# Performance work log

Hardware: AMD Instinct MI355X
Metric: run time of the kernel (lower is better)

## Reference

```python
import jax, jax.numpy as jnp
import numpy as np
from jax import lax

# Static problem sizes (see shape_source): 128 events x 512 points each
G, P, K = 128, 512, 16          # graphs, points per graph, knn k
FEAT = 128                       # n_samples*2
PLANES = [128, 96, 64, 32]       # linear reduction, n_graph=3, graph_out=32
N_OUT = 3                        # n_type


def setup_inputs() -> dict:
    key = jax.random.key(0)
    ks = jax.random.split(key, 24)
    N = G * P
    x = jax.random.normal(ks[0], (N, FEAT), jnp.float32)
    # coo: integer detector coords (cols 0,1) + graph id (col 2)
    xy = jax.random.randint(ks[1], (N, 2), 0, 32).astype(jnp.int32)
    gid = jnp.repeat(jnp.arange(G, dtype=jnp.int32), P)
    coo = jnp.concatenate([xy, gid[:, None]], axis=1)  # [N,3]
    inp = {"x": x, "coo": coo}
    # SAGEConv params per layer: lin_l (neighbor-mean path, with bias), lin_r (root path)
    ki = 2
    for l, (nin, nout) in enumerate(zip(PLANES[:-1], PLANES[1:])):
        s = 1.0 / np.sqrt(nin)
        inp[f"wl{l}"] = jax.random.normal(ks[ki], (nin, nout), jnp.float32) * s; ki += 1
        inp[f"wr{l}"] = jax.random.normal(ks[ki], (nin, nout), jnp.float32) * s; ki += 1
        inp[f"b{l}"] = jnp.zeros((nout,), jnp.float32)
    # MLP head: 32 -> 32 -> 3 with ReLU between (n_lin = 2)
    inp["lw0"] = jax.random.normal(ks[ki], (PLANES[-1], PLANES[-1]), jnp.float32) / np.sqrt(PLANES[-1]); ki += 1
    inp["lb0"] = jnp.zeros((PLANES[-1],), jnp.float32)
    inp["lw1"] = jax.random.normal(ks[ki], (PLANES[-1], N_OUT), jnp.float32) / np.sqrt(PLANES[-1]); ki += 1
    inp["lb1"] = jnp.zeros((N_OUT,), jnp.float32)
    return inp


def _knn_indices(coo):
    # knn_graph(coo, k, batch=coo[:,2], loop=False): k nearest within each graph,
    # self excluded. Batch segments are uniform size P so reshape per-graph.
    pos = coo.reshape(G, P, 3).astype(jnp.float32)
    d2 = jnp.sum((pos[:, :, None, :] - pos[:, None, :, :]) ** 2, axis=-1)  # [G,P,P]
    d2 = jnp.where(jnp.eye(P, dtype=bool), jnp.inf, d2)  # loop=False
    _, idx = lax.top_k(-d2, K)  # [G,P,K] neighbor (source) indices per target
    return idx


def reference(x, coo, wl0, wr0, b0, wl1, wr1, b1, wl2, wr2, b2, lw0, lb0, lw1, lb1):
    idx = _knn_indices(coo)
    h = x.reshape(G, P, FEAT)
    gather = jax.vmap(lambda hg, ig: hg[ig])  # per-graph neighbor gather
    for wl, wr, b in ((wl0, wr0, b0), (wl1, wr1, b1), (wl2, wr2, b2)):
        nbr_mean = gather(h, idx).mean(axis=2)  # [G,P,K,nin] -> [G,P,nin]
        # SAGEConv: lin_l(mean_j x_j) + lin_r(x_i), then ReLU (GraphLayer)
        h = jax.nn.relu(jnp.einsum('gpi,io->gpo', nbr_mean, wl)
                        + jnp.einsum('gpi,io->gpo', h, wr) + b)
    pooled = h.max(axis=1)  # global_max_pool over batch -> [G, 32]
    hid = jax.nn.relu(pooled @ lw0 + lb0)
    return hid @ lw1 + lb1  # [G, 3]
```

## Files before the change

kernel.cpp:

```cpp
#include <hip/hip_runtime.h>

#define G 128
#define P 512
#define K 16
#define NPTS (G * P)

typedef _Float16 half8 __attribute__((ext_vector_type(8)));
typedef float    floatx4 __attribute__((ext_vector_type(4)));

__device__ __forceinline__ unsigned uminu(unsigned a, unsigned b) { return a < b ? a : b; }

__device__ __forceinline__ void ce(unsigned& a, unsigned& b) {
    const unsigned lo = a < b ? a : b;
    const unsigned hi = a < b ? b : a;
    a = lo; b = hi;
}

__device__ __forceinline__ void sort16(unsigned k[16]) {
#pragma unroll
    for (int p = 1; p < 16; p <<= 1) {
#pragma unroll
        for (int q = p; q >= 1; q >>= 1) {
#pragma unroll
            for (int j = q % p; j + q < 16; j += 2 * q) {
#pragma unroll
                for (int i = 0; i < q; ++i) {
                    const int a = i + j, b2 = i + j + q;
                    if (b2 < 16 && (a / (2 * p)) == (b2 / (2 * p)))
                        ce(k[a], k[b2]);
                }
            }
        }
    }
}

__device__ __forceinline__ void halfmerge(unsigned best[16], const unsigned kb[16]) {
#pragma unroll
    for (int i = 0; i < 16; ++i) best[i] = uminu(best[i], kb[15 - i]);
#pragma unroll
    for (int d = 8; d >= 1; d >>= 1)
#pragma unroll
        for (int i = 0; i < 16; ++i)
            if ((i & d) == 0) ce(best[i], best[i + d]);
}

template <int KT, int NIN, int NOUT>
__device__ __forceinline__ void prep_elem(int e, const float* __restrict__ wl,
                                          const float* __restrict__ wr,
                                          _Float16* __restrict__ wf) {
    const int fr   = e >> 9;
    const int lane = (e >> 3) & 63;
    const int j    = e & 7;
    const int ntile = fr / KT;
    const int kt    = fr - ntile * KT;
    const int k = kt * 32 + ((lane >> 4) << 3) + j;
    const int n = ntile * 16 + (lane & 15);
    const float v = (k < NIN) ? wl[k * NOUT + n] : wr[(k - NIN) * NOUT + n];
    wf[e] = (_Float16)v;
}

__global__ __launch_bounds__(512, 4)
void pre_kernel(const int* __restrict__ coo, int* __restrict__ idx_out,
                const float* __restrict__ x, _Float16* __restrict__ x16,
                const float* __restrict__ wl0, const float* __restrict__ wr0,
                const float* __restrict__ wl1, const float* __restrict__ wr1,
                const float* __restrict__ wl2, const float* __restrict__ wr2,
                _Float16* __restrict__ wf0, _Float16* __restrict__ wf1,
                _Float16* __restrict__ wf2) {
    __shared__ float2 sxy[P];
    __shared__ unsigned mk[7][64][17];
    const int b   = blockIdx.x;
    const int tid = threadIdx.x;

    if (b < 1024) {
        const int g   = b >> 3;
        const int t0  = (b & 7) * 64;
        const int tgt = tid & 63;
        const int sub = tid >> 6;

        for (int i = tid; i < P; i += 512) {
            const int* cp = coo + (size_t)(g * P + i) * 3;
            sxy[i] = make_float2((float)cp[0], (float)cp[1]);
        }
        __syncthreads();

        const int tg = t0 + tgt;
        const float px = sxy[tg].x, py = sxy[tg].y;

        unsigned best[K];
#pragma unroll
        for (int k = 0; k < K; ++k) best[k] = 0xFFFFFFF0u + k;

        const int s0 = sub * 64;
#pragma unroll
        for (int batch = 0; batch < 4; ++batch) {
            unsigned kb[K];
#pragma unroll
            for (int j = 0; j < 16; ++j) {
                const int s = s0 + batch * 16 + j;
                const float2 c = sxy[s];
                const float dx = px - c.x, dy = py - c.y;
                const float keyf = fmaf(fmaf(dx, dx, dy * dy), 512.f, (float)s);
                unsigned key = (unsigned)keyf;
                if (s == tg) key = 0xFFFFFFFFu;
                kb[j] = key;
            }
            sort16(kb);
            halfmerge(best, kb);
        }

        if (sub != 0) {
#pragma unroll
            for (int k = 0; k < K; ++k) mk[sub - 1][tgt][k] = best[k];
        }
        __syncthreads();
        if (sub == 0) {
#pragma unroll 1
            for (int ss = 0; ss < 7; ++ss) {
                unsigned pb[K];
#pragma unroll
                for (int k = 0; k < K; ++k) pb[k] = mk[ss][tgt][k];
                halfmerge(best, pb);
            }
            int4* op = (int4*)(idx_out + (size_t)(g * P + tg) * K);
#pragma unroll
            for (int q4 = 0; q4 < 4; ++q4) {
                int4 o;
                o.x = (int)(best[q4 * 4 + 0] & (unsigned)(P - 1));
                o.y = (int)(best[q4 * 4 + 1] & (unsigned)(P - 1));
                o.z = (int)(best[q4 * 4 + 2] & (unsigned)(P - 1));
                o.w = (int)(best[q4 * 4 + 3] & (unsigned)(P - 1));
                op[q4] = o;
            }
        }
    } else if (b < 3072) {
        const int i = (b - 1024) * 512 + tid;
        const float4* p = (const float4*)(x + (size_t)i * 8);
        const float4 a = p[0], bq = p[1];
        half8 o;
        o[0] = (_Float16)a.x;  o[1] = (_Float16)a.y;
        o[2] = (_Float16)a.z;  o[3] = (_Float16)a.w;
        o[4] = (_Float16)bq.x; o[5] = (_Float16)bq.y;
        o[6] = (_Float16)bq.z; o[7] = (_Float16)bq.w;
        *(half8*)(x16 + (size_t)i * 8) = o;
    } else {
        const int e = (b - 3072) * 512 + tid;
        if (e < 24576)      prep_elem<8, 128, 96>(e,         wl0, wr0, wf0);
        else if (e < 36864) prep_elem<6,  96, 64>(e - 24576, wl1, wr1, wf1);
        else                prep_elem<4,  64, 32>(e - 36864, wl2, wr2, wf2);
    }
}

template <int CIN, int NOUT, bool POOL>
__global__ __launch_bounds__(256, 4)
void sage_kernel(const _Float16* __restrict__ hin, const int* __restrict__ idxg,
                 const _Float16* __restrict__ wf, const float* __restrict__ bias,
                 _Float16* __restrict__ hout, float* __restrict__ pool_part) {
    constexpr int KTm = CIN / 32;
    constexpr int KT  = CIN / 16;
    constexpr int NH  = NOUT / 32;
    constexpr int RS  = 136;

    __shared__ _Float16 As[64 * RS];

    const int tid  = threadIdx.x;
    const int b    = blockIdx.x;
    const int slot = b >> 3;
    const int g    = (b & 7) | ((slot & 15) << 3);
    const int chunk = slot >> 4;
    const int n0   = g * P + chunk * 64;
    const _Float16* __restrict__ hg = hin + (size_t)(g * P) * CIN;

    const int pt = tid >> 2;
    const int q  = tid & 3;

    const int4* ip = (const int4*)(idxg + (size_t)(n0 + pt) * K);
    const int4 na = ip[0], nb4 = ip[1], nc = ip[2], nd = ip[3];
    const int nn[16] = {na.x, na.y, na.z, na.w, nb4.x, nb4.y, nb4.z, nb4.w,
                        nc.x, nc.y, nc.z, nc.w, nd.x, nd.y, nd.z, nd.w};

#pragma unroll 1
    for (int c = 0; c < KTm; ++c) {
        const int ch = c * 32 + q * 8;
        half8 a0 = {}; half8 a1 = {};
#pragma unroll
        for (int k = 0; k < 16; k += 4) {
            const half8 v0 = *(const half8*)(hg + (size_t)nn[k + 0] * CIN + ch);
            const half8 v1 = *(const half8*)(hg + (size_t)nn[k + 1] * CIN + ch);
            const half8 v2 = *(const half8*)(hg + (size_t)nn[k + 2] * CIN + ch);
            const half8 v3 = *(const half8*)(hg + (size_t)nn[k + 3] * CIN + ch);
            a0 += v0; a1 += v1; a0 += v2; a1 += v3;
        }
        half8 m;
#pragma unroll
        for (int e = 0; e < 8; ++e)
            m[e] = (_Float16)(((float)a0[e] + (float)a1[e]) * 0.0625f);
        *(half8*)&As[pt * RS + (c * 4 + q) * 8] = m;
    }

    const int l  = tid & 63;
    const int wv = tid >> 6;
    const int mh = wv & 1;
    const int nh = wv >> 1;
    const int lm = l & 15, lq = l >> 4;

    float bs[NH];
#pragma unroll
    for (int nt = 0; nt < NH; ++nt)
        bs[nt] = bias[nh * (NOUT / 2) + nt * 16 + lm];

    __syncthreads();

    floatx4 acc[2][NH];
#pragma unroll
    for (int mt = 0; mt < 2; ++mt)
#pragma unroll
        for (int nt = 0; nt < NH; ++nt) {
            floatx4 z = {0.f, 0.f, 0.f, 0.f};
            acc[mt][nt] = z;
        }

#pragma unroll
    for (int kt = 0; kt < KT; ++kt) {
        half8 bfr[NH];
#pragma unroll
        for (int nt = 0; nt < NH; ++nt) {
            const int ng = nh * NH + nt;
            bfr[nt] = *(const half8*)(wf + ((size_t)(ng * KT + kt) * 64 + l) * 8);
        }
#pragma unroll
        for (int mt = 0; mt < 2; ++mt) {
            const int row = mh * 32 + mt * 16 + lm;
            half8 a;
            if (kt < KTm) {
                a = *(const half8*)&As[row * RS + (kt * 4 + lq) * 8];
            } else {
                a = *(const half8*)(hin + (size_t)(n0 + row) * CIN +
                                    (kt - KTm) * 32 + lq * 8);
            }
#pragma unroll
            for (int nt = 0; nt < NH; ++nt)
                acc[mt][nt] = __builtin_amdgcn_mfma_f32_16x16x32_f16(
                    a, bfr[nt], acc[mt][nt], 0, 0, 0);
        }
    }

    if constexpr (!POOL) {
#pragma unroll
        for (int mt = 0; mt < 2; ++mt)
#pragma unroll
            for (int nt = 0; nt < NH; ++nt) {
                const int n = nh * (NOUT / 2) + nt * 16 + lm;
#pragma unroll
                for (int r = 0; r < 4; ++r) {
                    const int p = n0 + mh * 32 + mt * 16 + lq * 4 + r;
                    float v = acc[mt][nt][r] + bs[nt];
                    v = v > 0.f ? v : 0.f;
                    hout[(size_t)p * NOUT + n] = (_Float16)v;
                }
            }
    } else {
        __shared__ float ps[4][16];
        float vmax = 0.f;
#pragma unroll
        for (int mt = 0; mt < 2; ++mt)
#pragma unroll
            for (int r = 0; r < 4; ++r)
                vmax = fmaxf(vmax, acc[mt][0][r] + bs[0]);
        vmax = fmaxf(vmax, __shfl_xor(vmax, 16, 64));
        vmax = fmaxf(vmax, __shfl_xor(vmax, 32, 64));
        if (lq == 0) ps[wv][lm] = vmax;
        __syncthreads();
        if (tid < 32) {
            const int nh2 = tid >> 4, lm2 = tid & 15;
            pool_part[(size_t)(g * 8 + chunk) * 32 + tid] =
                fmaxf(ps[nh2 * 2][lm2], ps[nh2 * 2 + 1][lm2]);
        }
    }
}

__global__ __launch_bounds__(64)
void head_kernel(const float* __restrict__ pool_part,
                 const float* __restrict__ lw0, const float* __restrict__ lb0,
                 const float* __restrict__ lw1, const float* __restrict__ lb1,
                 float* __restrict__ out) {
    __shared__ float pooled[32];
    __shared__ float hid[32];
    const int g = blockIdx.x;
    const int t = threadIdx.x;

    if (t < 32) {
        float m = pool_part[(size_t)(g * 8) * 32 + t];
#pragma unroll
        for (int c = 1; c < 8; ++c)
            m = fmaxf(m, pool_part[(size_t)(g * 8 + c) * 32 + t]);
        pooled[t] = m;
    }
    __syncthreads();
    if (t < 32) {
        float a = lb0[t];
#pragma unroll
        for (int i = 0; i < 32; ++i) a += pooled[i] * lw0[i * 32 + t];
        hid[t] = a > 0.f ? a : 0.f;
    }
    __syncthreads();
    if (t < 3) {
        float a = lb1[t];
#pragma unroll
        for (int i = 0; i < 32; ++i) a += hid[i] * lw1[i * 3 + t];
        out[g * 3 + t] = a;
    }
}

extern "C" void kernel_launch(void* const* d_in, const int* in_sizes, int n_in,
                              void* d_out, int out_size, void* d_ws, size_t ws_size,
                              hipStream_t stream) {
    const float* x   = (const float*)d_in[0];
    const int*   coo = (const int*)  d_in[1];
    const float* wl0 = (const float*)d_in[2];
    const float* wr0 = (const float*)d_in[3];
    const float* b0  = (const float*)d_in[4];
    const float* wl1 = (const float*)d_in[5];
    const float* wr1 = (const float*)d_in[6];
    const float* b1  = (const float*)d_in[7];
    const float* wl2 = (const float*)d_in[8];
    const float* wr2 = (const float*)d_in[9];
    const float* b2  = (const float*)d_in[10];
    const float* lw0 = (const float*)d_in[11];
    const float* lb0 = (const float*)d_in[12];
    const float* lw1 = (const float*)d_in[13];
    const float* lb1 = (const float*)d_in[14];
    float* out = (float*)d_out;

    char* ws = (char*)d_ws;
    _Float16* wf0 = (_Float16*)(ws + 0);
    _Float16* wf1 = (_Float16*)(ws + 49152);
    _Float16* wf2 = (_Float16*)(ws + 73728);
    int*      idx = (int*)     (ws + 81920);
    _Float16* x16 = (_Float16*)(ws + 4276224);
    _Float16* h1  = (_Float16*)(ws + 21053440);
    _Float16* h2  = (_Float16*)(ws + 33636352);
    float*    pool= (float*)   (ws + 42024960);

    pre_kernel<<<3152, 512, 0, stream>>>(coo, idx, x, x16,
                                         wl0, wr0, wl1, wr1, wl2, wr2,
                                         wf0, wf1, wf2);

    sage_kernel<128, 96, false><<<1024, 256, 0, stream>>>(x16, idx, wf0, b0, h1, nullptr);
    sage_kernel< 96, 64, false><<<1024, 256, 0, stream>>>(h1,  idx, wf1, b1, h2, nullptr);
    sage_kernel< 64, 32, true ><<<1024, 256, 0, stream>>>(h2,  idx, wf2, b2, nullptr, pool);

    head_kernel<<<G, 64, 0, stream>>>(pool, lw0, lb0, lw1, lb1, out);
}
```

Baseline: 162.5 us.

## Halve SAGE block tile to 32 points with 8 threads per point

Each SAGE block now handles 32 points instead of 64, with 8 threads per point splitting the channel groups during the neighbor-mean gather. Each wave owns a single 16-row MFMA tile. The grid doubles to 2048 blocks, launch bounds allow 8 blocks per CU, and pool partials grow to 16 chunks per graph. The aim is more parallelism and occupancy to hide gather latency. In exchange, weight fragments are reloaded twice as often per point and the per-thread work is smaller.

```diff
diff --git a/kernel.cpp b/kernel.cpp
--- a/kernel.cpp
+++ b/kernel.cpp
@@ -152,50 +152,55 @@
 }
 
 template <int CIN, int NOUT, bool POOL>
-__global__ __launch_bounds__(256, 4)
+__global__ __launch_bounds__(256, 8)
 void sage_kernel(const _Float16* __restrict__ hin, const int* __restrict__ idxg,
                  const _Float16* __restrict__ wf, const float* __restrict__ bias,
                  _Float16* __restrict__ hout, float* __restrict__ pool_part) {
     constexpr int KTm = CIN / 32;
     constexpr int KT  = CIN / 16;
     constexpr int NH  = NOUT / 32;
+    constexpr int NG  = CIN / 8;
+    constexpr int PASSES = (NG + 7) / 8;
     constexpr int RS  = 136;
 
-    __shared__ _Float16 As[64 * RS];
+    __shared__ _Float16 As[32 * RS];
 
     const int tid  = threadIdx.x;
     const int b    = blockIdx.x;
     const int slot = b >> 3;
     const int g    = (b & 7) | ((slot & 15) << 3);
     const int chunk = slot >> 4;
-    const int n0   = g * P + chunk * 64;
+    const int n0   = g * P + chunk * 32;
     const _Float16* __restrict__ hg = hin + (size_t)(g * P) * CIN;
 
-    const int pt = tid >> 2;
-    const int q  = tid & 3;
+    const int pt = tid >> 3;
+    const int q  = tid & 7;
 
     const int4* ip = (const int4*)(idxg + (size_t)(n0 + pt) * K);
     const int4 na = ip[0], nb4 = ip[1], nc = ip[2], nd = ip[3];
     const int nn[16] = {na.x, na.y, na.z, na.w, nb4.x, nb4.y, nb4.z, nb4.w,
                         nc.x, nc.y, nc.z, nc.w, nd.x, nd.y, nd.z, nd.w};
 
-#pragma unroll 1
-    for (int c = 0; c < KTm; ++c) {
-        const int ch = c * 32 + q * 8;
-        half8 a0 = {}; half8 a1 = {};
-#pragma unroll
-        for (int k = 0; k < 16; k += 4) {
-            const half8 v0 = *(const half8*)(hg + (size_t)nn[k + 0] * CIN + ch);
-            const half8 v1 = *(const half8*)(hg + (size_t)nn[k + 1] * CIN + ch);
-            const half8 v2 = *(const half8*)(hg + (size_t)nn[k + 2] * CIN + ch);
-            const half8 v3 = *(const half8*)(hg + (size_t)nn[k + 3] * CIN + ch);
-            a0 += v0; a1 += v1; a0 += v2; a1 += v3;
-        }
-        half8 m;
-#pragma unroll
-        for (int e = 0; e < 8; ++e)
-            m[e] = (_Float16)(((float)a0[e] + (float)a1[e]) * 0.0625f);
-        *(half8*)&As[pt * RS + (c * 4 + q) * 8] = m;
+#pragma unroll
+    for (int c = 0; c < PASSES; ++c) {
+        const int gi = c * 8 + q;
+        if (NG % 8 == 0 || gi < NG) {
+            const int ch = gi * 8;
+            half8 a0 = {}; half8 a1 = {};
+#pragma unroll
+            for (int k = 0; k < 16; k += 4) {
+                const half8 v0 = *(const half8*)(hg + (size_t)nn[k + 0] * CIN + ch);
+                const half8 v1 = *(const half8*)(hg + (size_t)nn[k + 1] * CIN + ch);
+                const half8 v2 = *(const half8*)(hg + (size_t)nn[k + 2] * CIN + ch);
+                const half8 v3 = *(const half8*)(hg + (size_t)nn[k + 3] * CIN + ch);
+                a0 += v0; a1 += v1; a0 += v2; a1 += v3;
+            }
+            half8 m;
+#pragma unroll
+            for (int e = 0; e < 8; ++e)
+                m[e] = (_Float16)(((float)a0[e] + (float)a1[e]) * 0.0625f);
+            *(half8*)&As[pt * RS + gi * 8] = m;
+        }
     }
 
     const int l  = tid & 63;
@@ -211,15 +216,14 @@
 
     __syncthreads();
 
-    floatx4 acc[2][NH];
-#pragma unroll
-    for (int mt = 0; mt < 2; ++mt)
-#pragma unroll
-        for (int nt = 0; nt < NH; ++nt) {
-            floatx4 z = {0.f, 0.f, 0.f, 0.f};
-            acc[mt][nt] = z;
-        }
-
+    floatx4 acc[NH];
+#pragma unroll
+    for (int nt = 0; nt < NH; ++nt) {
+        floatx4 z = {0.f, 0.f, 0.f, 0.f};
+        acc[nt] = z;
+    }
+
+    const int row = mh * 16 + lm;
 #pragma unroll
     for (int kt = 0; kt < KT; ++kt) {
         half8 bfr[NH];
@@ -228,52 +232,44 @@
             const int ng = nh * NH + nt;
             bfr[nt] = *(const half8*)(wf + ((size_t)(ng * KT + kt) * 64 + l) * 8);
         }
-#pragma unroll
-        for (int mt = 0; mt < 2; ++mt) {
-            const int row = mh * 32 + mt * 16 + lm;
-            half8 a;
-            if (kt < KTm) {
-                a = *(const half8*)&As[row * RS + (kt * 4 + lq) * 8];
-            } else {
-                a = *(const half8*)(hin + (size_t)(n0 + row) * CIN +
-                                    (kt - KTm) * 32 + lq * 8);
-            }
-#pragma unroll
-            for (int nt = 0; nt < NH; ++nt)
-                acc[mt][nt] = __builtin_amdgcn_mfma_f32_16x16x32_f16(
-                    a, bfr[nt], acc[mt][nt], 0, 0, 0);
-        }
+        half8 a;
+        if (kt < KTm) {
+            a = *(const half8*)&As[row * RS + (kt * 4 + lq) * 8];
+        } else {
+            a = *(const half8*)(hin + (size_t)(n0 + row) * CIN +
+                                (kt - KTm) * 32 + lq * 8);
+        }
+#pragma unroll
+        for (int nt = 0; nt < NH; ++nt)
+            acc[nt] = __builtin_amdgcn_mfma_f32_16x16x32_f16(
+                a, bfr[nt], acc[nt], 0, 0, 0);
     }
 
     if constexpr (!POOL) {
 #pragma unroll
-        for (int mt = 0; mt < 2; ++mt)
-#pragma unroll
-            for (int nt = 0; nt < NH; ++nt) {
-                const int n = nh * (NOUT / 2) + nt * 16 + lm;
-#pragma unroll
-                for (int r = 0; r < 4; ++r) {
-                    const int p = n0 + mh * 32 + mt * 16 + lq * 4 + r;
-                    float v = acc[mt][nt][r] + bs[nt];
-                    v = v > 0.f ? v : 0.f;
-                    hout[(size_t)p * NOUT + n] = (_Float16)v;
-                }
-            }
+        for (int nt = 0; nt < NH; ++nt) {
+            const int n = nh * (NOUT / 2) + nt * 16 + lm;
+#pragma unroll
+            for (int r = 0; r < 4; ++r) {
+                const int p = n0 + mh * 16 + lq * 4 + r;
+                float v = acc[nt][r] + bs[nt];
+                v = v > 0.f ? v : 0.f;
+                hout[(size_t)p * NOUT + n] = (_Float16)v;
+            }
+        }
     } else {
         __shared__ float ps[4][16];
         float vmax = 0.f;
 #pragma unroll
-        for (int mt = 0; mt < 2; ++mt)
-#pragma unroll
-            for (int r = 0; r < 4; ++r)
-                vmax = fmaxf(vmax, acc[mt][0][r] + bs[0]);
+        for (int r = 0; r < 4; ++r)
+            vmax = fmaxf(vmax, acc[0][r] + bs[0]);
         vmax = fmaxf(vmax, __shfl_xor(vmax, 16, 64));
         vmax = fmaxf(vmax, __shfl_xor(vmax, 32, 64));
         if (lq == 0) ps[wv][lm] = vmax;
         __syncthreads();
         if (tid < 32) {
             const int nh2 = tid >> 4, lm2 = tid & 15;
-            pool_part[(size_t)(g * 8 + chunk) * 32 + tid] =
+            pool_part[(size_t)(g * 16 + chunk) * 32 + tid] =
                 fmaxf(ps[nh2 * 2][lm2], ps[nh2 * 2 + 1][lm2]);
         }
     }
@@ -290,10 +286,10 @@
     const int t = threadIdx.x;
 
     if (t < 32) {
-        float m = pool_part[(size_t)(g * 8) * 32 + t];
-#pragma unroll
-        for (int c = 1; c < 8; ++c)
-            m = fmaxf(m, pool_part[(size_t)(g * 8 + c) * 32 + t]);
+        float m = pool_part[(size_t)(g * 16) * 32 + t];
+#pragma unroll
+        for (int c = 1; c < 16; ++c)
+            m = fmaxf(m, pool_part[(size_t)(g * 16 + c) * 32 + t]);
         pooled[t] = m;
     }
     __syncthreads();
@@ -346,9 +342,9 @@
                                          wl0, wr0, wl1, wr1, wl2, wr2,
                                          wf0, wf1, wf2);
 
-    sage_kernel<128, 96, false><<<1024, 256, 0, stream>>>(x16, idx, wf0, b0, h1, nullptr);
-    sage_kernel< 96, 64, false><<<1024, 256, 0, stream>>>(h1,  idx, wf1, b1, h2, nullptr);
-    sage_kernel< 64, 32, true ><<<1024, 256, 0, stream>>>(h2,  idx, wf2, b2, nullptr, pool);
+    sage_kernel<128, 96, false><<<NPTS / 32, 256, 0, stream>>>(x16, idx, wf0, b0, h1, nullptr);
+    sage_kernel< 96, 64, false><<<NPTS / 32, 256, 0, stream>>>(h1,  idx, wf1, b1, h2, nullptr);
+    sage_kernel< 64, 32, true ><<<NPTS / 32, 256, 0, stream>>>(h2,  idx, wf2, b2, nullptr, pool);
 
     head_kernel<<<G, 64, 0, stream>>>(pool, lw0, lb0, lw1, lb1, out);
 }
```

Result: slower. 169.5 us (+4.3%).
